# Kernel optimization log

Measured on AMD Instinct MI355X. Metric: run time of the kernel, lower is better.

The kernel has to match this reference:

```python
import jax, jax.numpy as jnp
import numpy as np

NUM_CODES = 1024
CODE_DIM = 256
COMMIT_W = 0.25
EPS = 1e-5
ENT_LO, ENT_HI = 0.5, 0.9
ENT_W = 0.1
VAR_FLOOR = 0.05
VAR_W = 1e-3
DECORR_W = 1e-3


def setup_inputs() -> dict:
    key = jax.random.key(0)
    k1, k2, k3 = jax.random.split(key, 3)
    inputs = jax.random.normal(k1, (16, 2048, CODE_DIM), dtype=jnp.float32)
    weight = jax.random.normal(k2, (NUM_CODES, CODE_DIM), dtype=jnp.float32) * 0.1
    usage_counts = jax.random.uniform(k3, (NUM_CODES,), dtype=jnp.float32)
    return {"inputs": inputs, "weight": weight, "usage_counts": usage_counts}


def reference(inputs, weight, usage_counts):
    K, D = weight.shape
    flat = inputs.reshape(-1, D)  # [N, D]
    # squared euclidean distances [N, K]
    dist = (flat ** 2).sum(axis=1, keepdims=True) - 2.0 * flat @ weight.T + (weight ** 2).sum(axis=1)
    idx = jnp.argmin(dist, axis=1)  # [N]
    quant = weight[idx].reshape(inputs.shape)

    commitment_loss = COMMIT_W * jnp.mean((jax.lax.stop_gradient(quant) - inputs) ** 2)
    # straight-through estimator
    quant_ste = inputs + jax.lax.stop_gradient(quant - inputs)

    # usage entropy regularizer
    probs = usage_counts + EPS
    probs = probs / jnp.maximum(probs.sum(), EPS * K)
    usage_entropy = -jnp.sum(probs * jnp.log(probs + EPS)) / np.log(float(K)).astype(np.float32)
    gap = jnp.where(usage_entropy < ENT_LO, ENT_LO - usage_entropy,
                    jnp.where(usage_entropy > ENT_HI, usage_entropy - ENT_HI, 0.0))
    entropy_loss = ENT_W * gap ** 2

    # variance floor penalty on codebook
    variance = jnp.var(weight, axis=0)
    variance_loss = VAR_W * jnp.mean(jax.nn.relu(VAR_FLOOR - variance))

    # decorrelation penalty
    wc = weight - weight.mean(axis=0, keepdims=True)
    cov = wc.T @ wc / float(K)  # [D, D]
    off_diag = cov - jnp.diag(jnp.diag(cov))
    decorrelation_loss = DECORR_W * jnp.mean(off_diag ** 2)

    total_loss = commitment_loss + entropy_loss + variance_loss + decorrelation_loss
    indices = idx.reshape(inputs.shape[:-1])
    return (quant_ste, indices, total_loss, commitment_loss, entropy_loss,
            variance_loss, decorrelation_loss, usage_entropy)
```

## Files before the change

kernel.cpp:

```cpp
#include <hip/hip_runtime.h>
#include <math.h>

#define DIMS   256
#define KCODES 1024
#define NTOT   32768
#define TAU    4.0e-4f

typedef __bf16 bf16x8 __attribute__((ext_vector_type(8)));
typedef float  f32x4  __attribute__((ext_vector_type(4)));

typedef const void __attribute__((address_space(1))) glb_cv;
typedef void __attribute__((address_space(3))) lds_v;

__device__ __forceinline__ void gload_lds16(const void* g, void* l) {
  __builtin_amdgcn_global_load_lds((glb_cv*)g, (lds_v*)l, 16, 0, 0);
}

#define WS_COMMIT   0
#define WS_FLAGCNT  1
#define WS_DECORR   2
#define WS_COLSUM   16
#define WS_COLSQ    272
#define WS_WSQ      1024
#define WS_XSQ      2048
#define WS_FLAGS    34816
#define WS_CAND1    67584
#define WS_CAND2    329728
#define WS_CANDI    591872
#define WS_WP       854016

#define OUT_Q    0
#define OUT_IDX  8388608
#define OUT_SCAL 8421376

__global__ __launch_bounds__(256) void prep_kernel(const float* __restrict__ X,
                                                   const float* __restrict__ W,
                                                   __bf16* __restrict__ Xp,
                                                   __bf16* __restrict__ Wp2,
                                                   float* ws) {
  int b = blockIdx.x;
  int tid = threadIdx.x;
  if (b < 512) {
    int row = b * 64 + (tid >> 2);
    int kg = tid & 3;
    int rb = row >> 7, rl = row & 127;
    int p1 = kg ^ (rl & 7);
    float sq = 0.f;
    #pragma unroll
    for (int kt = 0; kt < 8; kt++) {
      const float* s = X + (size_t)row * DIMS + kt * 32 + kg * 8;
      float4 u = *(const float4*)s;
      float4 v = *(const float4*)(s + 4);
      float f[8] = {u.x, u.y, u.z, u.w, v.x, v.y, v.z, v.w};
      bf16x8 hi, lo;
      #pragma unroll
      for (int e = 0; e < 8; e++) {
        __bf16 h = (__bf16)f[e];
        hi[e] = h;
        lo[e] = (__bf16)(f[e] - (float)h);
        sq = fmaf(f[e], f[e], sq);
      }
      size_t base = ((size_t)(rb * 8 + kt) * 128 + rl) * 64;
      *(bf16x8*)&Xp[base + p1 * 8] = hi;
      *(bf16x8*)&Xp[base + (p1 ^ 4) * 8] = lo;
    }
    sq += __shfl_xor(sq, 1);
    sq += __shfl_xor(sq, 2);
    if (kg == 0) ws[WS_XSQ + row] = sq;
  } else if (b < 544) {
    int b2 = b - 512;
    int g = b2 * 32 + (tid >> 3);
    int kt = tid & 7;
    int bn = g >> 7, c = g & 127;
    int wn = c >> 6, nt = (c >> 4) & 3, lcol = c & 15;
    size_t hibase = ((((size_t)(bn * 8 + kt) * 2 + wn) * 4 + nt) * 2 + 0) * 512;
    size_t lobase = hibase + 512;
    const float* s = W + (size_t)g * DIMS + kt * 32;
    float sq = 0.f;
    #pragma unroll
    for (int kq = 0; kq < 4; kq++) {
      float4 u = *(const float4*)(s + kq * 8);
      float4 v = *(const float4*)(s + kq * 8 + 4);
      float f[8] = {u.x, u.y, u.z, u.w, v.x, v.y, v.z, v.w};
      bf16x8 hi, lo;
      #pragma unroll
      for (int e = 0; e < 8; e++) {
        __bf16 h = (__bf16)f[e];
        hi[e] = h;
        lo[e] = (__bf16)(f[e] - (float)h);
        sq = fmaf(f[e], f[e], sq);
      }
      size_t off = (size_t)(kq * 16 + lcol) * 8;
      *(bf16x8*)&Wp2[hibase + off] = hi;
      *(bf16x8*)&Wp2[lobase + off] = lo;
    }
    sq += __shfl_xor(sq, 1);
    sq += __shfl_xor(sq, 2);
    sq += __shfl_xor(sq, 4);
    if (kt == 0) ws[WS_WSQ + g] = sq;
  } else {
    int d = tid;
    int r0 = (b - 544) * 128;
    float s = 0.f, sq = 0.f;
    #pragma unroll 8
    for (int k = 0; k < 128; k++) {
      float v = W[(size_t)(r0 + k) * DIMS + d];
      s += v;
      sq = fmaf(v, v, sq);
    }
    atomicAdd(&ws[WS_COLSUM + d], s);
    atomicAdd(&ws[WS_COLSQ + d], sq);
  }
}

__global__ __launch_bounds__(256, 3) void pass1_kernel(const __bf16* __restrict__ Xp,
                                                       const __bf16* __restrict__ Wp2,
                                                       float* ws) {
  __shared__ __align__(16) char asmem[32768];
  __shared__ float wsqs[128];
  __shared__ float d1L[256];
  __shared__ float d2L[256];
  __shared__ int   i1L[256];

  int tid = threadIdx.x;
  int lane = tid & 63, wave = tid >> 6;
  int waveM = wave >> 1, waveN = wave & 1;
  int quad = lane >> 4, col = lane & 15;
  int l = blockIdx.x;
  int bm = (l & 7) * 32 + ((l >> 3) & 31);
  int bn = l >> 8;
  int rowBase = bm * 128, cb = bn * 128;

  if (tid < 128) wsqs[tid] = ws[WS_WSQ + cb + tid];

  f32x4 acc[4][4];
  #pragma unroll
  for (int i = 0; i < 4; i++)
    #pragma unroll
    for (int j = 0; j < 4; j++) acc[i][j] = (f32x4){0.f, 0.f, 0.f, 0.f};

  const char* abase = (const char*)(Xp + ((size_t)(bm * 8) << 13));
  const __bf16* wbase = Wp2 + ((size_t)(bn * 8) * 2 + waveN) * 4096;

  #pragma unroll
  for (int i = 0; i < 4; i++) {
    int off = wave * 4096 + i * 1024;
    gload_lds16(abase + off + lane * 16, asmem + off);
  }

  for (int kt = 0; kt < 8; kt++) {
    __syncthreads();
    const __bf16* wp = wbase + (size_t)kt * 8192;
    bf16x8 bfr[8];
    #pragma unroll
    for (int f = 0; f < 8; f++) bfr[f] = *(const bf16x8*)(wp + f * 512 + lane * 8);
    if (kt < 7) {
      const char* as = abase + (size_t)(kt + 1) * 16384;
      int bsel = (kt + 1) & 1;
      #pragma unroll
      for (int i = 0; i < 4; i++) {
        int off = wave * 4096 + i * 1024;
        gload_lds16(as + off + lane * 16, asmem + bsel * 16384 + off);
      }
    }
    const __bf16* Ab = (const __bf16*)(asmem + (kt & 1) * 16384);
    bf16x8 ah[4], al[4];
    #pragma unroll
    for (int mt = 0; mt < 4; mt++) {
      int r = waveM * 64 + mt * 16 + col;
      int ph = quad ^ (r & 7);
      ah[mt] = *(const bf16x8*)&Ab[r * 64 + ph * 8];
      al[mt] = *(const bf16x8*)&Ab[r * 64 + (ph ^ 4) * 8];
    }
    #pragma unroll
    for (int nt = 0; nt < 4; nt++) {
      #pragma unroll
      for (int mt = 0; mt < 4; mt++) {
        acc[mt][nt] = __builtin_amdgcn_mfma_f32_16x16x32_bf16(ah[mt], bfr[nt * 2], acc[mt][nt], 0, 0, 0);
        acc[mt][nt] = __builtin_amdgcn_mfma_f32_16x16x32_bf16(ah[mt], bfr[nt * 2 + 1], acc[mt][nt], 0, 0, 0);
        acc[mt][nt] = __builtin_amdgcn_mfma_f32_16x16x32_bf16(al[mt], bfr[nt * 2], acc[mt][nt], 0, 0, 0);
      }
    }
  }

  #pragma unroll
  for (int mt = 0; mt < 4; mt++) {
    #pragma unroll
    for (int r = 0; r < 4; r++) {
      float d1 = 3.0e38f, d2 = 3.0e38f;
      int i1 = 0;
      #pragma unroll
      for (int nt = 0; nt < 4; nt++) {
        int lc = waveN * 64 + nt * 16 + col;
        float d = wsqs[lc] - 2.0f * acc[mt][nt][r];
        int g = cb + lc;
        if (d < d1) { d2 = d1; d1 = d; i1 = g; }
        else if (d < d2) d2 = d;
      }
      #pragma unroll
      for (int m = 1; m < 16; m <<= 1) {
        float od1 = __shfl_xor(d1, m);
        int oi1 = __shfl_xor(i1, m);
        float od2 = __shfl_xor(d2, m);
        if (od1 < d1 || (od1 == d1 && oi1 < i1)) {
          d2 = fminf(d1, fminf(d2, od2));
          d1 = od1; i1 = oi1;
        } else {
          d2 = fminf(od1, fminf(d2, od2));
        }
      }
      if (col == 0) {
        int lr = waveM * 64 + mt * 16 + quad * 4 + r;
        d1L[lr * 2 + waveN] = d1;
        d2L[lr * 2 + waveN] = d2;
        i1L[lr * 2 + waveN] = i1;
      }
    }
  }
  __syncthreads();
  if (tid < 128) {
    float a1 = d1L[tid * 2], a2 = d2L[tid * 2];
    int ai = i1L[tid * 2];
    float b1 = d1L[tid * 2 + 1], b2 = d2L[tid * 2 + 1];
    int bi = i1L[tid * 2 + 1];
    float m1, m2; int mi;
    if (b1 < a1 || (b1 == a1 && bi < ai)) { m1 = b1; mi = bi; m2 = fminf(a1, b2); }
    else { m1 = a1; mi = ai; m2 = fminf(b1, a2); }
    int o = bn * NTOT + rowBase + tid;
    ws[WS_CAND1 + o] = m1;
    ws[WS_CAND2 + o] = m2;
    ((int*)ws)[WS_CANDI + o] = mi;
  }
}

__global__ __launch_bounds__(256) void pass2_kernel(const float* __restrict__ W,
                                                    float* __restrict__ outQ,
                                                    float* __restrict__ outIdx, float* ws) {
  __shared__ int idx_s[256];
  int tid = threadIdx.x;
  int row = blockIdx.x * 256 + tid;
  const float* c1 = ws + WS_CAND1;
  const float* c2 = ws + WS_CAND2;
  const int* ci = (const int*)ws + WS_CANDI;
  float m1 = 3.0e38f, m2 = 3.0e38f;
  int mi = 0;
  #pragma unroll
  for (int b = 0; b < 8; b++) {
    int o = b * NTOT + row;
    float b1 = c1[o], b2 = c2[o];
    int bi = ci[o];
    if (b1 < m1 || (b1 == m1 && bi < mi)) { m2 = fminf(m1, b2); m1 = b1; mi = bi; }
    else { m2 = fminf(m2, b1); }
  }
  outIdx[row] = (float)mi;
  idx_s[tid] = mi;
  int* wsI = (int*)ws;
  if (m2 - m1 < TAU) {
    int p = atomicAdd(&wsI[WS_FLAGCNT], 1);
    wsI[WS_FLAGS + p] = row;
  }
  float partial = ws[WS_XSQ + row] + m1;
  #pragma unroll
  for (int m = 32; m >= 1; m >>= 1) partial += __shfl_xor(partial, m);
  if ((tid & 63) == 0) atomicAdd(&ws[WS_COMMIT], partial);
  __syncthreads();
  int wave = tid >> 6, lane = tid & 63;
  int rowBase = blockIdx.x * 256;
  #pragma unroll 4
  for (int i = 0; i < 64; i++) {
    int rl = wave * 64 + i;
    int ix = idx_s[rl];
    float4 v = ((const float4*)(W + (size_t)ix * DIMS))[lane];
    ((float4*)(outQ + (size_t)(rowBase + rl) * DIMS))[lane] = v;
  }
}

__global__ __launch_bounds__(256) void cov_kernel(const float* __restrict__ W, float* ws) {
  __shared__ float wi_s[4][KCODES];
  __shared__ float red[4];
  int tid = threadIdx.x;
  int i0 = blockIdx.x * 4;
  int rr = tid >> 2, c = tid & 3;
  #pragma unroll
  for (int b = 0; b < 16; b++) {
    int row = b * 64 + rr;
    wi_s[c][row] = W[(size_t)row * DIMS + i0 + c];
  }
  __syncthreads();
  int j = tid;
  float a0 = 0.f, a1 = 0.f, a2 = 0.f, a3 = 0.f;
  for (int k = 0; k < KCODES; k += 4) {
    #pragma unroll
    for (int u = 0; u < 4; u++) {
      float wj = W[(size_t)(k + u) * DIMS + j];
      a0 = fmaf(wi_s[0][k + u], wj, a0);
      a1 = fmaf(wi_s[1][k + u], wj, a1);
      a2 = fmaf(wi_s[2][k + u], wj, a2);
      a3 = fmaf(wi_s[3][k + u], wj, a3);
    }
  }
  const float inv = 1.0f / 1024.0f;
  float mj = ws[WS_COLSUM + j] * inv;
  float dots[4] = {a0, a1, a2, a3};
  float v = 0.f;
  #pragma unroll
  for (int r = 0; r < 4; r++) {
    float mi = ws[WS_COLSUM + i0 + r] * inv;
    float cc = dots[r] * inv - mi * mj;
    if (i0 + r != j) v = fmaf(cc, cc, v);
  }
  #pragma unroll
  for (int m = 32; m >= 1; m >>= 1) v += __shfl_xor(v, m);
  if ((j & 63) == 0) red[j >> 6] = v;
  __syncthreads();
  if (j == 0) atomicAdd(&ws[WS_DECORR], (red[0] + red[1]) + (red[2] + red[3]));
}

__global__ __launch_bounds__(256) void refine_kernel(const float* __restrict__ X,
                                                     const float* __restrict__ W,
                                                     float* __restrict__ outQ,
                                                     float* __restrict__ outIdx, float* ws) {
  __shared__ float xs[DIMS];
  __shared__ double dm[256];
  __shared__ int im[256];
  __shared__ int chosen;
  const int* wsI = (const int*)ws;
  int cnt = wsI[WS_FLAGCNT];
  const int* list = wsI + WS_FLAGS;
  int tid = threadIdx.x;
  for (int f = blockIdx.x; f < cnt; f += gridDim.x) {
    int row = list[f];
    __syncthreads();
    if (tid < 64) ((float4*)xs)[tid] = ((const float4*)(X + (size_t)row * DIMS))[tid];
    __syncthreads();
    double bd = 1.0e300;
    int bi = 0;
    for (int jj = 0; jj < 4; jj++) {
      int c = tid + 256 * jj;
      double a0 = 0.0, a1 = 0.0, a2 = 0.0, a3 = 0.0;
      const float* wr = W + (size_t)c * DIMS;
      #pragma unroll 4
      for (int d4 = 0; d4 < 64; d4++) {
        float4 w = ((const float4*)wr)[d4];
        float4 x = ((const float4*)xs)[d4];
        double e0 = (double)x.x - (double)w.x;
        double e1 = (double)x.y - (double)w.y;
        double e2 = (double)x.z - (double)w.z;
        double e3 = (double)x.w - (double)w.w;
        a0 += e0 * e0; a1 += e1 * e1; a2 += e2 * e2; a3 += e3 * e3;
      }
      double s = (a0 + a1) + (a2 + a3);
      if (s < bd) { bd = s; bi = c; }
    }
    dm[tid] = bd; im[tid] = bi;
    __syncthreads();
    for (int st = 128; st >= 1; st >>= 1) {
      if (tid < st) {
        if (dm[tid + st] < dm[tid] || (dm[tid + st] == dm[tid] && im[tid + st] < im[tid])) {
          dm[tid] = dm[tid + st]; im[tid] = im[tid + st];
        }
      }
      __syncthreads();
    }
    if (tid == 0) { chosen = im[0]; outIdx[row] = (float)im[0]; }
    __syncthreads();
    int ix = chosen;
    if (tid < 64)
      ((float4*)(outQ + (size_t)row * DIMS))[tid] = ((const float4*)(W + (size_t)ix * DIMS))[tid];
  }
}

__global__ __launch_bounds__(256) void finalize_kernel(const float* __restrict__ U, float* ws,
                                                       float* __restrict__ out) {
  __shared__ float red[256];
  int tid = threadIdx.x;
  float s = 0.f;
  for (int e = tid; e < KCODES; e += 256) s += U[e] + 1e-5f;
  red[tid] = s;
  __syncthreads();
  for (int st = 128; st >= 1; st >>= 1) {
    if (tid < st) red[tid] += red[tid + st];
    __syncthreads();
  }
  float S = red[0];
  __syncthreads();
  float denom = fmaxf(S, 1e-5f * 1024.0f);
  float h = 0.f;
  for (int e = tid; e < KCODES; e += 256) {
    float p = (U[e] + 1e-5f) / denom;
    h += p * logf(p + 1e-5f);
  }
  red[tid] = h;
  __syncthreads();
  for (int st = 128; st >= 1; st >>= 1) {
    if (tid < st) red[tid] += red[tid + st];
    __syncthreads();
  }
  float H = -red[0] / 6.93147180559945f;
  __syncthreads();
  float m = ws[WS_COLSUM + tid] * (1.0f / 1024.0f);
  float var = ws[WS_COLSQ + tid] * (1.0f / 1024.0f) - m * m;
  float r = 0.05f - var;
  red[tid] = r > 0.f ? r : 0.f;
  __syncthreads();
  for (int st = 128; st >= 1; st >>= 1) {
    if (tid < st) red[tid] += red[tid + st];
    __syncthreads();
  }
  if (tid == 0) {
    float varloss = 1e-3f * (red[0] / 256.0f);
    float gap = H < 0.5f ? (0.5f - H) : (H > 0.9f ? (H - 0.9f) : 0.0f);
    float entloss = 0.1f * gap * gap;
    float commit = 0.25f * ws[WS_COMMIT] / 8388608.0f;
    float dec = 1e-3f * ws[WS_DECORR] / 65536.0f;
    float* sc = out + OUT_SCAL;
    sc[0] = commit + entloss + varloss + dec;
    sc[1] = commit;
    sc[2] = entloss;
    sc[3] = varloss;
    sc[4] = dec;
    sc[5] = H;
  }
}

extern "C" void kernel_launch(void* const* d_in, const int* in_sizes, int n_in, void* d_out,
                              int out_size, void* d_ws, size_t ws_size, hipStream_t stream) {
  const float* X = (const float*)d_in[0];
  const float* W = (const float*)d_in[1];
  const float* U = (const float*)d_in[2];
  float* out = (float*)d_out;
  float* ws = (float*)d_ws;
  __bf16* Xp = (__bf16*)(out + OUT_Q);
  __bf16* Wp2 = (__bf16*)(ws + WS_WP);

  hipMemsetAsync(d_ws, 0, 2112, stream);
  prep_kernel<<<552, 256, 0, stream>>>(X, W, Xp, Wp2, ws);
  pass1_kernel<<<2048, 256, 0, stream>>>(Xp, Wp2, ws);
  pass2_kernel<<<NTOT / 256, 256, 0, stream>>>(W, out + OUT_Q, out + OUT_IDX, ws);
  cov_kernel<<<64, 256, 0, stream>>>(W, ws);
  refine_kernel<<<512, 256, 0, stream>>>(X, W, out + OUT_Q, out + OUT_IDX, ws);
  finalize_kernel<<<1, 256, 0, stream>>>(U, ws, out);
}
```

Measured before the change: 246.2 us.

## Load MFMA operands directly from global, merge cov/finalize into other kernels

The GEMM pass now reads pre-packed X fragments straight into registers with double buffering, instead of staging through LDS with global_load_lds. To support this, the prep kernel packs X in the same fragment layout as W. The covariance computation moves into extra prep blocks that compute their own column means, and finalize moves into an extra refine block, removing two launches. Risks include higher register pressure (occupancy hint lowered to 2), atomic row-norm accumulation needing a larger memset, and finalize possibly racing with refine, though it only reads values already complete.

```diff
diff --git a/kernel.cpp b/kernel.cpp
--- a/kernel.cpp
+++ b/kernel.cpp
@@ -8,13 +8,6 @@
 
 typedef __bf16 bf16x8 __attribute__((ext_vector_type(8)));
 typedef float  f32x4  __attribute__((ext_vector_type(4)));
-
-typedef const void __attribute__((address_space(1))) glb_cv;
-typedef void __attribute__((address_space(3))) lds_v;
-
-__device__ __forceinline__ void gload_lds16(const void* g, void* l) {
-  __builtin_amdgcn_global_load_lds((glb_cv*)g, (lds_v*)l, 16, 0, 0);
-}
 
 #define WS_COMMIT   0
 #define WS_FLAGCNT  1
@@ -33,6 +26,7 @@
 #define OUT_IDX  8388608
 #define OUT_SCAL 8421376
 
+
 __global__ __launch_bounds__(256) void prep_kernel(const float* __restrict__ X,
                                                    const float* __restrict__ W,
                                                    __bf16* __restrict__ Xp,
@@ -40,17 +34,23 @@
                                                    float* ws) {
   int b = blockIdx.x;
   int tid = threadIdx.x;
-  if (b < 512) {
-    int row = b * 64 + (tid >> 2);
-    int kg = tid & 3;
-    int rb = row >> 7, rl = row & 127;
-    int p1 = kg ^ (rl & 7);
+  if (b < 1056) {
+    bool isW = b >= 1024;
+    const float* src = isW ? W : X;
+    __bf16* dst = isW ? Wp2 : Xp;
+    int sqoff = isW ? WS_WSQ : WS_XSQ;
+    int bb = isW ? b - 1024 : b;
+    int kt = tid >> 5, mtl = (tid >> 4) & 1, lc = tid & 15;
+    int row = bb * 32 + mtl * 16 + lc;
+    int bt = row >> 7, c = row & 127;
+    int wv = c >> 6, t = (c >> 4) & 3;
+    size_t hibase = ((((size_t)(bt * 8 + kt) * 2 + wv) * 4 + t) * 2) * 512;
+    const float* s = src + (size_t)row * DIMS + kt * 32;
     float sq = 0.f;
     #pragma unroll
-    for (int kt = 0; kt < 8; kt++) {
-      const float* s = X + (size_t)row * DIMS + kt * 32 + kg * 8;
-      float4 u = *(const float4*)s;
-      float4 v = *(const float4*)(s + 4);
+    for (int kq = 0; kq < 4; kq++) {
+      float4 u = *(const float4*)(s + kq * 8);
+      float4 v = *(const float4*)(s + kq * 8 + 4);
       float f[8] = {u.x, u.y, u.z, u.w, v.x, v.y, v.z, v.w};
       bf16x8 hi, lo;
       #pragma unroll
@@ -60,47 +60,14 @@
         lo[e] = (__bf16)(f[e] - (float)h);
         sq = fmaf(f[e], f[e], sq);
       }
-      size_t base = ((size_t)(rb * 8 + kt) * 128 + rl) * 64;
-      *(bf16x8*)&Xp[base + p1 * 8] = hi;
-      *(bf16x8*)&Xp[base + (p1 ^ 4) * 8] = lo;
-    }
-    sq += __shfl_xor(sq, 1);
-    sq += __shfl_xor(sq, 2);
-    if (kg == 0) ws[WS_XSQ + row] = sq;
-  } else if (b < 544) {
-    int b2 = b - 512;
-    int g = b2 * 32 + (tid >> 3);
-    int kt = tid & 7;
-    int bn = g >> 7, c = g & 127;
-    int wn = c >> 6, nt = (c >> 4) & 3, lcol = c & 15;
-    size_t hibase = ((((size_t)(bn * 8 + kt) * 2 + wn) * 4 + nt) * 2 + 0) * 512;
-    size_t lobase = hibase + 512;
-    const float* s = W + (size_t)g * DIMS + kt * 32;
-    float sq = 0.f;
-    #pragma unroll
-    for (int kq = 0; kq < 4; kq++) {
-      float4 u = *(const float4*)(s + kq * 8);
-      float4 v = *(const float4*)(s + kq * 8 + 4);
-      float f[8] = {u.x, u.y, u.z, u.w, v.x, v.y, v.z, v.w};
-      bf16x8 hi, lo;
-      #pragma unroll
-      for (int e = 0; e < 8; e++) {
-        __bf16 h = (__bf16)f[e];
-        hi[e] = h;
-        lo[e] = (__bf16)(f[e] - (float)h);
-        sq = fmaf(f[e], f[e], sq);
-      }
-      size_t off = (size_t)(kq * 16 + lcol) * 8;
-      *(bf16x8*)&Wp2[hibase + off] = hi;
-      *(bf16x8*)&Wp2[lobase + off] = lo;
-    }
-    sq += __shfl_xor(sq, 1);
-    sq += __shfl_xor(sq, 2);
-    sq += __shfl_xor(sq, 4);
-    if (kt == 0) ws[WS_WSQ + g] = sq;
-  } else {
+      size_t off = (size_t)(kq * 16 + lc) * 8;
+      *(bf16x8*)&dst[hibase + off] = hi;
+      *(bf16x8*)&dst[hibase + 512 + off] = lo;
+    }
+    atomicAdd(&ws[sqoff + row], sq);
+  } else if (b < 1064) {
     int d = tid;
-    int r0 = (b - 544) * 128;
+    int r0 = (b - 1056) * 128;
     float s = 0.f, sq = 0.f;
     #pragma unroll 8
     for (int k = 0; k < 128; k++) {
@@ -110,13 +77,59 @@
     }
     atomicAdd(&ws[WS_COLSUM + d], s);
     atomicAdd(&ws[WS_COLSQ + d], sq);
+  } else {
+    __shared__ float wi_s[2][KCODES];
+    __shared__ float red2[256];
+    __shared__ float mi_s[2];
+    __shared__ float red[4];
+    int i0 = (b - 1064) * 2;
+    int rr = tid >> 1, cc = tid & 1;
+    #pragma unroll
+    for (int q = 0; q < 8; q++) {
+      int row = q * 128 + rr;
+      wi_s[cc][row] = W[(size_t)row * DIMS + i0 + cc];
+    }
+    __syncthreads();
+    float pm = 0.f;
+    #pragma unroll
+    for (int q = 0; q < 8; q++) pm += wi_s[cc][rr * 8 + q];
+    red2[tid] = pm;
+    __syncthreads();
+    if (tid < 2) {
+      float s = 0.f;
+      for (int k = tid; k < 256; k += 2) s += red2[k];
+      mi_s[tid] = s * (1.0f / 1024.0f);
+    }
+    int j = tid;
+    float a0 = 0.f, a1 = 0.f, sj = 0.f;
+    for (int k = 0; k < KCODES; k += 4) {
+      #pragma unroll
+      for (int u = 0; u < 4; u++) {
+        float wj = W[(size_t)(k + u) * DIMS + j];
+        a0 = fmaf(wi_s[0][k + u], wj, a0);
+        a1 = fmaf(wi_s[1][k + u], wj, a1);
+        sj += wj;
+      }
+    }
+    __syncthreads();
+    const float inv = 1.0f / 1024.0f;
+    float mj = sj * inv;
+    float v = 0.f;
+    float c0 = a0 * inv - mi_s[0] * mj;
+    if (i0 != j) v = fmaf(c0, c0, v);
+    float c1 = a1 * inv - mi_s[1] * mj;
+    if (i0 + 1 != j) v = fmaf(c1, c1, v);
+    #pragma unroll
+    for (int m = 32; m >= 1; m >>= 1) v += __shfl_xor(v, m);
+    if ((j & 63) == 0) red[j >> 6] = v;
+    __syncthreads();
+    if (j == 0) atomicAdd(&ws[WS_DECORR], (red[0] + red[1]) + (red[2] + red[3]));
   }
 }
 
-__global__ __launch_bounds__(256, 3) void pass1_kernel(const __bf16* __restrict__ Xp,
+__global__ __launch_bounds__(256, 2) void pass1_kernel(const __bf16* __restrict__ Xp,
                                                        const __bf16* __restrict__ Wp2,
                                                        float* ws) {
-  __shared__ __align__(16) char asmem[32768];
   __shared__ float wsqs[128];
   __shared__ float d1L[256];
   __shared__ float d2L[256];
@@ -124,7 +137,7 @@
 
   int tid = threadIdx.x;
   int lane = tid & 63, wave = tid >> 6;
-  int waveM = wave >> 1, waveN = wave & 1;
+  int wm = wave >> 1, wn = wave & 1;
   int quad = lane >> 4, col = lane & 15;
   int l = blockIdx.x;
   int bm = (l & 7) * 32 + ((l >> 3) & 31);
@@ -139,49 +152,42 @@
     #pragma unroll
     for (int j = 0; j < 4; j++) acc[i][j] = (f32x4){0.f, 0.f, 0.f, 0.f};
 
-  const char* abase = (const char*)(Xp + ((size_t)(bm * 8) << 13));
-  const __bf16* wbase = Wp2 + ((size_t)(bn * 8) * 2 + waveN) * 4096;
-
-  #pragma unroll
-  for (int i = 0; i < 4; i++) {
-    int off = wave * 4096 + i * 1024;
-    gload_lds16(abase + off + lane * 16, asmem + off);
-  }
-
+  const bf16x8* ab = (const bf16x8*)(Xp + (size_t)bm * 65536 + wm * 4096) + lane;
+  const bf16x8* bb = (const bf16x8*)(Wp2 + (size_t)bn * 65536 + wn * 4096) + lane;
+
+  bf16x8 Af[2][8], Bf[2][8];
+  #pragma unroll
+  for (int f = 0; f < 4; f++) {
+    Af[0][f * 2] = ab[f * 128];
+    Af[0][f * 2 + 1] = ab[f * 128 + 64];
+    Bf[0][f * 2] = bb[f * 128];
+    Bf[0][f * 2 + 1] = bb[f * 128 + 64];
+  }
+  #pragma unroll
   for (int kt = 0; kt < 8; kt++) {
-    __syncthreads();
-    const __bf16* wp = wbase + (size_t)kt * 8192;
-    bf16x8 bfr[8];
-    #pragma unroll
-    for (int f = 0; f < 8; f++) bfr[f] = *(const bf16x8*)(wp + f * 512 + lane * 8);
+    const int cur = kt & 1, nxt = cur ^ 1;
     if (kt < 7) {
-      const char* as = abase + (size_t)(kt + 1) * 16384;
-      int bsel = (kt + 1) & 1;
-      #pragma unroll
-      for (int i = 0; i < 4; i++) {
-        int off = wave * 4096 + i * 1024;
-        gload_lds16(as + off + lane * 16, asmem + bsel * 16384 + off);
-      }
-    }
-    const __bf16* Ab = (const __bf16*)(asmem + (kt & 1) * 16384);
-    bf16x8 ah[4], al[4];
-    #pragma unroll
-    for (int mt = 0; mt < 4; mt++) {
-      int r = waveM * 64 + mt * 16 + col;
-      int ph = quad ^ (r & 7);
-      ah[mt] = *(const bf16x8*)&Ab[r * 64 + ph * 8];
-      al[mt] = *(const bf16x8*)&Ab[r * 64 + (ph ^ 4) * 8];
+      const bf16x8* an = ab + (kt + 1) * 1024;
+      const bf16x8* bv = bb + (kt + 1) * 1024;
+      #pragma unroll
+      for (int f = 0; f < 4; f++) {
+        Af[nxt][f * 2] = an[f * 128];
+        Af[nxt][f * 2 + 1] = an[f * 128 + 64];
+        Bf[nxt][f * 2] = bv[f * 128];
+        Bf[nxt][f * 2 + 1] = bv[f * 128 + 64];
+      }
     }
     #pragma unroll
     for (int nt = 0; nt < 4; nt++) {
       #pragma unroll
       for (int mt = 0; mt < 4; mt++) {
-        acc[mt][nt] = __builtin_amdgcn_mfma_f32_16x16x32_bf16(ah[mt], bfr[nt * 2], acc[mt][nt], 0, 0, 0);
-        acc[mt][nt] = __builtin_amdgcn_mfma_f32_16x16x32_bf16(ah[mt], bfr[nt * 2 + 1], acc[mt][nt], 0, 0, 0);
-        acc[mt][nt] = __builtin_amdgcn_mfma_f32_16x16x32_bf16(al[mt], bfr[nt * 2], acc[mt][nt], 0, 0, 0);
-      }
-    }
-  }
+        acc[mt][nt] = __builtin_amdgcn_mfma_f32_16x16x32_bf16(Af[cur][mt * 2], Bf[cur][nt * 2], acc[mt][nt], 0, 0, 0);
+        acc[mt][nt] = __builtin_amdgcn_mfma_f32_16x16x32_bf16(Af[cur][mt * 2], Bf[cur][nt * 2 + 1], acc[mt][nt], 0, 0, 0);
+        acc[mt][nt] = __builtin_amdgcn_mfma_f32_16x16x32_bf16(Af[cur][mt * 2 + 1], Bf[cur][nt * 2], acc[mt][nt], 0, 0, 0);
+      }
+    }
+  }
+  __syncthreads();
 
   #pragma unroll
   for (int mt = 0; mt < 4; mt++) {
@@ -191,7 +197,7 @@
       int i1 = 0;
       #pragma unroll
       for (int nt = 0; nt < 4; nt++) {
-        int lc = waveN * 64 + nt * 16 + col;
+        int lc = wn * 64 + nt * 16 + col;
         float d = wsqs[lc] - 2.0f * acc[mt][nt][r];
         int g = cb + lc;
         if (d < d1) { d2 = d1; d1 = d; i1 = g; }
@@ -210,10 +216,10 @@
         }
       }
       if (col == 0) {
-        int lr = waveM * 64 + mt * 16 + quad * 4 + r;
-        d1L[lr * 2 + waveN] = d1;
-        d2L[lr * 2 + waveN] = d2;
-        i1L[lr * 2 + waveN] = i1;
+        int lr = wm * 64 + mt * 16 + quad * 4 + r;
+        d1L[lr * 2 + wn] = d1;
+        d2L[lr * 2 + wn] = d2;
+        i1L[lr * 2 + wn] = i1;
       }
     }
   }
@@ -275,60 +281,72 @@
   }
 }
 
-__global__ __launch_bounds__(256) void cov_kernel(const float* __restrict__ W, float* ws) {
-  __shared__ float wi_s[4][KCODES];
-  __shared__ float red[4];
-  int tid = threadIdx.x;
-  int i0 = blockIdx.x * 4;
-  int rr = tid >> 2, c = tid & 3;
-  #pragma unroll
-  for (int b = 0; b < 16; b++) {
-    int row = b * 64 + rr;
-    wi_s[c][row] = W[(size_t)row * DIMS + i0 + c];
-  }
-  __syncthreads();
-  int j = tid;
-  float a0 = 0.f, a1 = 0.f, a2 = 0.f, a3 = 0.f;
-  for (int k = 0; k < KCODES; k += 4) {
-    #pragma unroll
-    for (int u = 0; u < 4; u++) {
-      float wj = W[(size_t)(k + u) * DIMS + j];
-      a0 = fmaf(wi_s[0][k + u], wj, a0);
-      a1 = fmaf(wi_s[1][k + u], wj, a1);
-      a2 = fmaf(wi_s[2][k + u], wj, a2);
-      a3 = fmaf(wi_s[3][k + u], wj, a3);
-    }
-  }
-  const float inv = 1.0f / 1024.0f;
-  float mj = ws[WS_COLSUM + j] * inv;
-  float dots[4] = {a0, a1, a2, a3};
-  float v = 0.f;
-  #pragma unroll
-  for (int r = 0; r < 4; r++) {
-    float mi = ws[WS_COLSUM + i0 + r] * inv;
-    float cc = dots[r] * inv - mi * mj;
-    if (i0 + r != j) v = fmaf(cc, cc, v);
-  }
-  #pragma unroll
-  for (int m = 32; m >= 1; m >>= 1) v += __shfl_xor(v, m);
-  if ((j & 63) == 0) red[j >> 6] = v;
-  __syncthreads();
-  if (j == 0) atomicAdd(&ws[WS_DECORR], (red[0] + red[1]) + (red[2] + red[3]));
-}
-
 __global__ __launch_bounds__(256) void refine_kernel(const float* __restrict__ X,
                                                      const float* __restrict__ W,
                                                      float* __restrict__ outQ,
-                                                     float* __restrict__ outIdx, float* ws) {
+                                                     float* __restrict__ outIdx, float* ws,
+                                                     const float* __restrict__ U,
+                                                     float* __restrict__ out) {
   __shared__ float xs[DIMS];
   __shared__ double dm[256];
   __shared__ int im[256];
   __shared__ int chosen;
+  int tid = threadIdx.x;
+  if (blockIdx.x == 512) {
+    __shared__ float red[256];
+    float s = 0.f;
+    for (int e = tid; e < KCODES; e += 256) s += U[e] + 1e-5f;
+    red[tid] = s;
+    __syncthreads();
+    for (int st = 128; st >= 1; st >>= 1) {
+      if (tid < st) red[tid] += red[tid + st];
+      __syncthreads();
+    }
+    float S = red[0];
+    __syncthreads();
+    float denom = fmaxf(S, 1e-5f * 1024.0f);
+    float h = 0.f;
+    for (int e = tid; e < KCODES; e += 256) {
+      float p = (U[e] + 1e-5f) / denom;
+      h += p * logf(p + 1e-5f);
+    }
+    red[tid] = h;
+    __syncthreads();
+    for (int st = 128; st >= 1; st >>= 1) {
+      if (tid < st) red[tid] += red[tid + st];
+      __syncthreads();
+    }
+    float H = -red[0] / 6.93147180559945f;
+    __syncthreads();
+    float m = ws[WS_COLSUM + tid] * (1.0f / 1024.0f);
+    float var = ws[WS_COLSQ + tid] * (1.0f / 1024.0f) - m * m;
+    float r = 0.05f - var;
+    red[tid] = r > 0.f ? r : 0.f;
+    __syncthreads();
+    for (int st = 128; st >= 1; st >>= 1) {
+      if (tid < st) red[tid] += red[tid + st];
+      __syncthreads();
+    }
+    if (tid == 0) {
+      float varloss = 1e-3f * (red[0] / 256.0f);
+      float gap = H < 0.5f ? (0.5f - H) : (H > 0.9f ? (H - 0.9f) : 0.0f);
+      float entloss = 0.1f * gap * gap;
+      float commit = 0.25f * ws[WS_COMMIT] / 8388608.0f;
+      float dec = 1e-3f * ws[WS_DECORR] / 65536.0f;
+      float* sc = out + OUT_SCAL;
+      sc[0] = commit + entloss + varloss + dec;
+      sc[1] = commit;
+      sc[2] = entloss;
+      sc[3] = varloss;
+      sc[4] = dec;
+      sc[5] = H;
+    }
+    return;
+  }
   const int* wsI = (const int*)ws;
   int cnt = wsI[WS_FLAGCNT];
   const int* list = wsI + WS_FLAGS;
-  int tid = threadIdx.x;
-  for (int f = blockIdx.x; f < cnt; f += gridDim.x) {
+  for (int f = blockIdx.x; f < cnt; f += 512) {
     int row = list[f];
     __syncthreads();
     if (tid < 64) ((float4*)xs)[tid] = ((const float4*)(X + (size_t)row * DIMS))[tid];
@@ -370,59 +388,6 @@
   }
 }
 
-__global__ __launch_bounds__(256) void finalize_kernel(const float* __restrict__ U, float* ws,
-                                                       float* __restrict__ out) {
-  __shared__ float red[256];
-  int tid = threadIdx.x;
-  float s = 0.f;
-  for (int e = tid; e < KCODES; e += 256) s += U[e] + 1e-5f;
-  red[tid] = s;
-  __syncthreads();
-  for (int st = 128; st >= 1; st >>= 1) {
-    if (tid < st) red[tid] += red[tid + st];
-    __syncthreads();
-  }
-  float S = red[0];
-  __syncthreads();
-  float denom = fmaxf(S, 1e-5f * 1024.0f);
-  float h = 0.f;
-  for (int e = tid; e < KCODES; e += 256) {
-    float p = (U[e] + 1e-5f) / denom;
-    h += p * logf(p + 1e-5f);
-  }
-  red[tid] = h;
-  __syncthreads();
-  for (int st = 128; st >= 1; st >>= 1) {
-    if (tid < st) red[tid] += red[tid + st];
-    __syncthreads();
-  }
-  float H = -red[0] / 6.93147180559945f;
-  __syncthreads();
-  float m = ws[WS_COLSUM + tid] * (1.0f / 1024.0f);
-  float var = ws[WS_COLSQ + tid] * (1.0f / 1024.0f) - m * m;
-  float r = 0.05f - var;
-  red[tid] = r > 0.f ? r : 0.f;
-  __syncthreads();
-  for (int st = 128; st >= 1; st >>= 1) {
-    if (tid < st) red[tid] += red[tid + st];
-    __syncthreads();
-  }
-  if (tid == 0) {
-    float varloss = 1e-3f * (red[0] / 256.0f);
-    float gap = H < 0.5f ? (0.5f - H) : (H > 0.9f ? (H - 0.9f) : 0.0f);
-    float entloss = 0.1f * gap * gap;
-    float commit = 0.25f * ws[WS_COMMIT] / 8388608.0f;
-    float dec = 1e-3f * ws[WS_DECORR] / 65536.0f;
-    float* sc = out + OUT_SCAL;
-    sc[0] = commit + entloss + varloss + dec;
-    sc[1] = commit;
-    sc[2] = entloss;
-    sc[3] = varloss;
-    sc[4] = dec;
-    sc[5] = H;
-  }
-}
-
 extern "C" void kernel_launch(void* const* d_in, const int* in_sizes, int n_in, void* d_out,
                               int out_size, void* d_ws, size_t ws_size, hipStream_t stream) {
   const float* X = (const float*)d_in[0];
@@ -433,11 +398,9 @@
   __bf16* Xp = (__bf16*)(out + OUT_Q);
   __bf16* Wp2 = (__bf16*)(ws + WS_WP);
 
-  hipMemsetAsync(d_ws, 0, 2112, stream);
-  prep_kernel<<<552, 256, 0, stream>>>(X, W, Xp, Wp2, ws);
+  hipMemsetAsync(d_ws, 0, 139264, stream);
+  prep_kernel<<<1192, 256, 0, stream>>>(X, W, Xp, Wp2, ws);
   pass1_kernel<<<2048, 256, 0, stream>>>(Xp, Wp2, ws);
   pass2_kernel<<<NTOT / 256, 256, 0, stream>>>(W, out + OUT_Q, out + OUT_IDX, ws);
-  cov_kernel<<<64, 256, 0, stream>>>(W, ws);
-  refine_kernel<<<512, 256, 0, stream>>>(X, W, out + OUT_Q, out + OUT_IDX, ws);
-  finalize_kernel<<<1, 256, 0, stream>>>(U, ws, out);
+  refine_kernel<<<513, 256, 0, stream>>>(X, W, out + OUT_Q, out + OUT_IDX, ws, U, out);
 }
```

New measurement: 237.8 us. -3.4%, faster.
